# Performance work log

Hardware: AMD Instinct MI355X
Metric: run time of the kernel (lower is better)

Reference implementation:

```python
import jax, jax.numpy as jnp
import numpy as np

NEG_SLOPE = 0.01  # torch nn.LeakyReLU default


def setup_inputs() -> dict:
    key = jax.random.key(0)
    k1, k2, k3 = jax.random.split(key, 3)
    B, N, D = 16, 1024, 256
    i_em = jax.random.normal(k1, (B, N, D), dtype=jnp.float32)
    # att_a: Linear(2D -> 1); weight flattened to [2D], scalar bias [1]
    a_w = jax.random.normal(k2, (2 * D,), dtype=jnp.float32) * (1.0 / np.sqrt(2 * D))
    a_b = jax.random.normal(k3, (1,), dtype=jnp.float32) * 0.01
    return {"i_em": i_em, "a_w": a_w, "a_b": a_b}


def reference(i_em, a_w, a_b):
    # Original: cat(query_i, key_j) @ a_w + b over all (i, j) pairs, which
    # splits algebraically: score[b,i,j] = i_em[b,i] @ a_w[:D] + i_em[b,j] @ a_w[D:] + b
    D = i_em.shape[-1]
    aq, ak = a_w[:D], a_w[D:]
    q = jnp.einsum('bnd,d->bn', i_em, aq)  # [B, N]
    k = jnp.einsum('bnd,d->bn', i_em, ak)  # [B, N]
    scores = q[:, :, None] + k[:, None, :] + a_b[0]  # [B, N, N]
    scores = jnp.where(scores >= 0, scores, NEG_SLOPE * scores)  # LeakyReLU
    # dropout is identity in eval mode
    alphas = jax.nn.softmax(scores, axis=-1)  # over key dim j
    return alphas[..., None]  # [B, N, N, 1]
```

## Files before the change

### kernel.cpp

```cpp
#include <hip/hip_runtime.h>
#include <hip/hip_bf16.h>

#define NEG_SLOPE 0.01f

#define B_DIM 16
#define N_DIM 1024
#define D_DIM 256
#define ROWS (B_DIM * N_DIM)

typedef float fvec4 __attribute__((ext_vector_type(4)));

__device__ __forceinline__ float wave_reduce_sum(float v) {
#pragma unroll
    for (int off = 32; off > 0; off >>= 1) v += __shfl_xor(v, off, 64);
    return v;
}

__global__ __launch_bounds__(256) void qk_kernel(const float* __restrict__ i_em,
                                                 const float* __restrict__ a_w,
                                                 float* __restrict__ q,
                                                 float* __restrict__ k) {
    const int wave = threadIdx.x >> 6;
    const int lane = threadIdx.x & 63;
    const int row  = blockIdx.x * 4 + wave;

    const float4 e  = *reinterpret_cast<const float4*>(i_em + (size_t)row * D_DIM + lane * 4);
    const float4 wq = *reinterpret_cast<const float4*>(a_w + lane * 4);
    const float4 wk = *reinterpret_cast<const float4*>(a_w + D_DIM + lane * 4);

    float sq = e.x * wq.x + e.y * wq.y + e.z * wq.z + e.w * wq.w;
    float sk = e.x * wk.x + e.y * wk.y + e.z * wk.z + e.w * wk.w;

    sq = wave_reduce_sum(sq);
    sk = wave_reduce_sum(sk);

    if (lane == 0) {
        q[row] = sq;
        k[row] = sk;
    }
}

__global__ __launch_bounds__(256) void softmax_kernel(const float* __restrict__ q,
                                                      const float* __restrict__ k,
                                                      const float* __restrict__ a_b,
                                                      float* __restrict__ out) {
    const int wid  = threadIdx.x >> 6;
    const int lane = threadIdx.x & 63;
    const int row0 = blockIdx.x * 8 + wid * 2;
    const int b    = row0 >> 10;

    const float4* k4 = reinterpret_cast<const float4*>(k + b * N_DIM);
    float4 kv[4];
#pragma unroll
    for (int c = 0; c < 4; ++c) kv[c] = k4[c * 64 + lane];

    const float bias = a_b[0];

#pragma unroll
    for (int r = 0; r < 2; ++r) {
        const int row = row0 + r;
        const float qi = q[row] + bias;

        float e[4][4];
        float s = 0.0f;
#pragma unroll
        for (int c = 0; c < 4; ++c) {
            float v0 = qi + kv[c].x; v0 = (v0 >= 0.0f) ? v0 : NEG_SLOPE * v0;
            float v1 = qi + kv[c].y; v1 = (v1 >= 0.0f) ? v1 : NEG_SLOPE * v1;
            float v2 = qi + kv[c].z; v2 = (v2 >= 0.0f) ? v2 : NEG_SLOPE * v2;
            float v3 = qi + kv[c].w; v3 = (v3 >= 0.0f) ? v3 : NEG_SLOPE * v3;
            e[c][0] = __expf(v0);
            e[c][1] = __expf(v1);
            e[c][2] = __expf(v2);
            e[c][3] = __expf(v3);
            s += (e[c][0] + e[c][1]) + (e[c][2] + e[c][3]);
        }
        s = wave_reduce_sum(s);
        const float inv = __builtin_amdgcn_rcpf(s);

        fvec4* o4 = reinterpret_cast<fvec4*>(out + (size_t)row * N_DIM);
#pragma unroll
        for (int c = 0; c < 4; ++c) {
            fvec4 o;
            o.x = e[c][0] * inv;
            o.y = e[c][1] * inv;
            o.z = e[c][2] * inv;
            o.w = e[c][3] * inv;
            __builtin_nontemporal_store(o, &o4[c * 64 + lane]);
        }
    }
}

extern "C" void kernel_launch(void* const* d_in, const int* in_sizes, int n_in,
                              void* d_out, int out_size, void* d_ws, size_t ws_size,
                              hipStream_t stream) {
    const float* i_em = (const float*)d_in[0];
    const float* a_w  = (const float*)d_in[1];
    const float* a_b  = (const float*)d_in[2];
    float* out = (float*)d_out;

    float* q = (float*)d_ws;
    float* k = q + ROWS;

    qk_kernel<<<ROWS / 4, 256, 0, stream>>>(i_em, a_w, q, k);
    softmax_kernel<<<ROWS / 8, 256, 0, stream>>>(q, k, a_b, out);
}
```

Measured before the change: 22.27 us.

## Fuse q/k projection and softmax into one cooperative kernel with grid sync

Merges the projection kernel and the softmax kernel into a single persistent cooperative launch of 1024 blocks. Each wave computes q and k for 4 rows, folds the bias into q, does a grid-wide sync, then writes softmax output for the same rows. The intent is to remove the second launch and the gap between kernels. In exchange it pays for a grid barrier and the cooperative launch path, and it needs all 1024 blocks resident at once.

```diff
diff --git a/kernel.cpp b/kernel.cpp
--- a/kernel.cpp
+++ b/kernel.cpp
@@ -1,5 +1,6 @@
 #include <hip/hip_runtime.h>
 #include <hip/hip_bf16.h>
+#include <hip/hip_cooperative_groups.h>
 
 #define NEG_SLOPE 0.01f
 
@@ -7,6 +8,10 @@
 #define N_DIM 1024
 #define D_DIM 256
 #define ROWS (B_DIM * N_DIM)
+
+#define GRID_BLOCKS 1024
+#define ROWS_PER_BLOCK (ROWS / GRID_BLOCKS)
+#define ROWS_PER_WAVE  (ROWS_PER_BLOCK / 4)
 
 typedef float fvec4 __attribute__((ext_vector_type(4)));
 
@@ -16,37 +21,45 @@
     return v;
 }
 
-__global__ __launch_bounds__(256) void qk_kernel(const float* __restrict__ i_em,
-                                                 const float* __restrict__ a_w,
-                                                 float* __restrict__ q,
-                                                 float* __restrict__ k) {
-    const int wave = threadIdx.x >> 6;
+__global__ __launch_bounds__(256, 4) void fused_kernel(const float* __restrict__ i_em,
+                                                       const float* __restrict__ a_w,
+                                                       const float* __restrict__ a_b,
+                                                       float* __restrict__ qb,
+                                                       float* __restrict__ k,
+                                                       float* __restrict__ out) {
+    const int wid  = threadIdx.x >> 6;
     const int lane = threadIdx.x & 63;
-    const int row  = blockIdx.x * 4 + wave;
 
-    const float4 e  = *reinterpret_cast<const float4*>(i_em + (size_t)row * D_DIM + lane * 4);
     const float4 wq = *reinterpret_cast<const float4*>(a_w + lane * 4);
     const float4 wk = *reinterpret_cast<const float4*>(a_w + D_DIM + lane * 4);
+    const float bias = a_b[0];
 
-    float sq = e.x * wq.x + e.y * wq.y + e.z * wq.z + e.w * wq.w;
-    float sk = e.x * wk.x + e.y * wk.y + e.z * wk.z + e.w * wk.w;
+    const int arow0 = blockIdx.x * ROWS_PER_BLOCK + wid * ROWS_PER_WAVE;
 
-    sq = wave_reduce_sum(sq);
-    sk = wave_reduce_sum(sk);
+    float sq[ROWS_PER_WAVE], sk[ROWS_PER_WAVE];
+#pragma unroll
+    for (int r = 0; r < ROWS_PER_WAVE; ++r) {
+        const fvec4 e = __builtin_nontemporal_load(
+            reinterpret_cast<const fvec4*>(i_em + (size_t)(arow0 + r) * D_DIM + lane * 4));
+        sq[r] = e.x * wq.x + e.y * wq.y + e.z * wq.z + e.w * wq.w;
+        sk[r] = e.x * wk.x + e.y * wk.y + e.z * wk.z + e.w * wk.w;
+    }
+#pragma unroll
+    for (int r = 0; r < ROWS_PER_WAVE; ++r) {
+        sq[r] = wave_reduce_sum(sq[r]);
+        sk[r] = wave_reduce_sum(sk[r]);
+    }
+    if (lane == 0) {
+#pragma unroll
+        for (int r = 0; r < ROWS_PER_WAVE; ++r) {
+            qb[arow0 + r] = sq[r] + bias;
+            k[arow0 + r]  = sk[r];
+        }
+    }
 
-    if (lane == 0) {
-        q[row] = sq;
-        k[row] = sk;
-    }
-}
+    cooperative_groups::this_grid().sync();
 
-__global__ __launch_bounds__(256) void softmax_kernel(const float* __restrict__ q,
-                                                      const float* __restrict__ k,
-                                                      const float* __restrict__ a_b,
-                                                      float* __restrict__ out) {
-    const int wid  = threadIdx.x >> 6;
-    const int lane = threadIdx.x & 63;
-    const int row0 = blockIdx.x * 8 + wid * 2;
+    const int row0 = arow0;
     const int b    = row0 >> 10;
 
     const float4* k4 = reinterpret_cast<const float4*>(k + b * N_DIM);
@@ -54,12 +67,10 @@
 #pragma unroll
     for (int c = 0; c < 4; ++c) kv[c] = k4[c * 64 + lane];
 
-    const float bias = a_b[0];
-
 #pragma unroll
-    for (int r = 0; r < 2; ++r) {
+    for (int r = 0; r < ROWS_PER_WAVE; ++r) {
         const int row = row0 + r;
-        const float qi = q[row] + bias;
+        const float qi = qb[row];
 
         float e[4][4];
         float s = 0.0f;
@@ -99,9 +110,11 @@
     const float* a_b  = (const float*)d_in[2];
     float* out = (float*)d_out;
 
-    float* q = (float*)d_ws;
-    float* k = q + ROWS;
+    float* qb = (float*)d_ws;
+    float* k  = qb + ROWS;
 
-    qk_kernel<<<ROWS / 4, 256, 0, stream>>>(i_em, a_w, q, k);
-    softmax_kernel<<<ROWS / 8, 256, 0, stream>>>(q, k, a_b, out);
+    void* args[] = {(void*)&i_em, (void*)&a_w, (void*)&a_b,
+                    (void*)&qb, (void*)&k, (void*)&out};
+    hipLaunchCooperativeKernel(reinterpret_cast<void*>(fused_kernel),
+                               dim3(GRID_BLOCKS), dim3(256), args, 0, stream);
 }
```

New measurement: 74.23 us. +233.3%, slower.
